# Performance work log

Measured on AMD Instinct MI355X. Metric: run time of the kernel, lower is better.

Reference implementation:

```python
import jax, jax.numpy as jnp
import numpy as np

N_PE = 100000   # num 'pe' nodes
N_R = 100000    # num 'router' nodes
E = 600000      # edges per relation
D_IN = 64       # input feature dim per node type
H = 128         # hidden_channels
G = 64          # graphs in batch


def setup_inputs() -> dict:
    key = jax.random.key(0)
    ks = jax.random.split(key, 20)
    inp = {}
    inp["x_pe"] = jax.random.normal(ks[0], (N_PE, D_IN), jnp.float32)
    inp["x_r"] = jax.random.normal(ks[1], (N_R, D_IN), jnp.float32)
    # edge_index per relation: row0 = src node ids, row1 = dst node ids
    inp["ei_per"] = jax.random.randint(ks[2], (2, E), 0, N_PE, jnp.int32)   # pe -> router
    inp["ei_rpe"] = jax.random.randint(ks[3], (2, E), 0, N_R, jnp.int32)    # router -> pe
    inp["ei_rr"] = jax.random.randint(ks[4], (2, E), 0, N_R, jnp.int32)     # router -> router
    inp["batch_pe"] = jnp.sort(jax.random.randint(ks[5], (N_PE,), 0, G, jnp.int32))
    inp["batch_r"] = jnp.sort(jax.random.randint(ks[6], (N_R,), 0, G, jnp.int32))
    # GraphConv params, relation axis ordered [pe->router, router->pe, router->router]
    s1 = 1.0 / np.sqrt(D_IN)
    s2 = 1.0 / np.sqrt(H)
    inp["Wrel1"] = jax.random.normal(ks[7], (3, D_IN, H), jnp.float32) * s1
    inp["brel1"] = jnp.zeros((3, H), jnp.float32)
    inp["Wroot1"] = jax.random.normal(ks[8], (3, D_IN, H), jnp.float32) * s1
    inp["Wrel23"] = jax.random.normal(ks[9], (2, 3, H, H), jnp.float32) * s2
    inp["brel23"] = jnp.zeros((2, 3, H), jnp.float32)
    inp["Wroot23"] = jax.random.normal(ks[10], (2, 3, H, H), jnp.float32) * s2
    # per-node-type MLP heads, type axis ordered [pe, router]
    inp["mlp_W1"] = jax.random.normal(ks[11], (2, H, 5), jnp.float32) * s2
    inp["mlp_b1"] = jnp.zeros((2, 5), jnp.float32)
    inp["mlp_W2"] = jax.random.normal(ks[12], (2, 5, 1), jnp.float32) * (1.0 / np.sqrt(5.0))
    inp["mlp_b2"] = jnp.zeros((2, 1), jnp.float32)
    inp["out_W"] = jax.random.normal(ks[13], (2, 1), jnp.float32) * (1.0 / np.sqrt(2.0))
    inp["out_b"] = jnp.zeros((1,), jnp.float32)
    return inp


def _hetero_graphconv(x_pe, x_r, ei_per, ei_rpe, ei_rr, Wrel, brel, Wroot):
    # GraphConv: lin_rel(scatter_add(x_src)) + lin_root(x_dst); to_hetero sums per dst type.
    agg_r_from_pe = jax.ops.segment_sum(x_pe[ei_per[0]], ei_per[1], num_segments=N_R)
    agg_pe_from_r = jax.ops.segment_sum(x_r[ei_rpe[0]], ei_rpe[1], num_segments=N_PE)
    agg_r_from_r = jax.ops.segment_sum(x_r[ei_rr[0]], ei_rr[1], num_segments=N_R)
    o_pe = agg_pe_from_r @ Wrel[1] + brel[1] + x_pe @ Wroot[1]
    o_r = (agg_r_from_pe @ Wrel[0] + brel[0] + x_r @ Wroot[0]) \
        + (agg_r_from_r @ Wrel[2] + brel[2] + x_r @ Wroot[2])
    return o_pe, o_r


def reference(x_pe, x_r, ei_per, ei_rpe, ei_rr, batch_pe, batch_r,
              Wrel1, brel1, Wroot1, Wrel23, brel23, Wroot23,
              mlp_W1, mlp_b1, mlp_W2, mlp_b2, out_W, out_b):
    h_pe, h_r = _hetero_graphconv(x_pe, x_r, ei_per, ei_rpe, ei_rr, Wrel1, brel1, Wroot1)
    h_pe, h_r = jax.nn.relu(h_pe), jax.nn.relu(h_r)
    h_pe, h_r = _hetero_graphconv(h_pe, h_r, ei_per, ei_rpe, ei_rr, Wrel23[0], brel23[0], Wroot23[0])
    h_pe, h_r = jax.nn.relu(h_pe), jax.nn.relu(h_r)
    h_pe, h_r = _hetero_graphconv(h_pe, h_r, ei_per, ei_rpe, ei_rr, Wrel23[1], brel23[1], Wroot23[1])
    gm_pe = jax.ops.segment_max(h_pe, batch_pe, num_segments=G)  # [G, H]
    gm_r = jax.ops.segment_max(h_r, batch_r, num_segments=G)
    def mlp(x, W1, b1, W2, b2):
        return jax.nn.relu(x @ W1 + b1) @ W2 + b2
    o_pe = mlp(gm_pe, mlp_W1[0], mlp_b1[0], mlp_W2[0], mlp_b2[0])  # [G, 1]
    o_r = mlp(gm_r, mlp_W1[1], mlp_b1[1], mlp_W2[1], mlp_b2[1])
    cat = jnp.concatenate([o_pe, o_r], axis=1)  # [G, 2]
    return cat @ out_W + out_b  # [G, 1]
```

## Files before the change

kernel.cpp:

```cpp
#include <hip/hip_runtime.h>
#include <cstddef>
#include <cstdint>

#define DIN 64
#define HID 128
#define NBKMAX 256
#define EPB 2048

typedef _Float16 half4v __attribute__((ext_vector_type(4)));
typedef _Float16 half8v __attribute__((ext_vector_type(8)));
typedef float f32x16 __attribute__((ext_vector_type(16)));

__device__ __forceinline__ unsigned encf(float f) {
    unsigned b = __float_as_uint(f);
    return (b & 0x80000000u) ? ~b : (b | 0x80000000u);
}
__device__ __forceinline__ float decf(unsigned u) {
    unsigned b = (u & 0x80000000u) ? (u & 0x7FFFFFFFu) : ~u;
    return __uint_as_float(b);
}

__global__ void conv_x2_k(const float* s0, _Float16* d0, int n40,
                          const float* s1, _Float16* d1, int n41) {
    int r = blockIdx.y;
    const float* s = r == 0 ? s0 : s1;
    _Float16* d = r == 0 ? d0 : d1;
    int n4 = r == 0 ? n40 : n41;
    int i = blockIdx.x * 256 + threadIdx.x;
    if (i >= n4) return;
    float4 v = *reinterpret_cast<const float4*>(&s[i * 4]);
    half4v h;
    h.x = (_Float16)v.x; h.y = (_Float16)v.y; h.z = (_Float16)v.z; h.w = (_Float16)v.w;
    *reinterpret_cast<half4v*>(&d[i * 4]) = h;
}

struct CW { const float* src; const float* src2; _Float16* dst; int K; int total; };
__global__ __launch_bounds__(256) void prep_k(
    CW c0, CW c1, CW c2, CW c3, CW c4, CW c5, CW c6, CW c7,
    const int* e0, const int* e1, const int* e2, int E,
    int* hc0, int* hc1, int* hc2,
    const int* bpe, int npe, int* spe,
    const int* brr, int nrr, int* srr, int G) {
    int y = blockIdx.y;
    if (y < 8) {
        CW J;
        switch (y) {
            case 0: J = c0; break; case 1: J = c1; break; case 2: J = c2; break;
            case 3: J = c3; break; case 4: J = c4; break; case 5: J = c5; break;
            case 6: J = c6; break; default: J = c7; break;
        }
        int i = blockIdx.x * 256 + threadIdx.x;
        if (i >= J.total) return;
        int m = i / (J.K * HID);
        int rem = i % (J.K * HID);
        int k = rem / HID;
        int col = rem % HID;
        float v = J.src[i];
        if (J.src2) v += J.src2[i];
        J.dst[(size_t)m * HID * J.K + (size_t)col * J.K + k] = (_Float16)v;
    } else if (y < 11) {
        int r = y - 8;
        const int* ei = r == 0 ? e0 : (r == 1 ? e1 : e2);
        int* cnt = r == 0 ? hc0 : (r == 1 ? hc1 : hc2);
        __shared__ int sc[NBKMAX];
        int t = threadIdx.x;
        sc[t] = 0;
        __syncthreads();
        int base = blockIdx.x * EPB;
        if (base >= E) return;
        int n = min(EPB, E - base);
        for (int i = t; i < n; i += 256)
            atomicAdd(&sc[(unsigned)ei[E + base + i] >> 9], 1);
        __syncthreads();
        if (sc[t]) atomicAdd(&cnt[t], sc[t]);
    } else {
        int r = blockIdx.x;
        if (r >= 2) return;
        const int* batch = r == 0 ? bpe : brr;
        int n = r == 0 ? npe : nrr;
        int* starts = r == 0 ? spe : srr;
        int g = threadIdx.x;
        if (g > G) return;
        int lo = 0, hi = n;
        while (lo < hi) {
            int mid = (lo + hi) >> 1;
            if (batch[mid] < g) lo = mid + 1; else hi = mid;
        }
        starts[g] = lo;
    }
}

__global__ __launch_bounds__(256) void bscan_k(int* c0, int* bb0, int* cu0, int* rp0, int n0,
                                               int* c1, int* bb1, int* cu1, int* rp1, int n1,
                                               int* c2, int* bb2, int* cu2, int* rp2, int n2,
                                               int E) {
    __shared__ int sh[256];
    int t = threadIdx.x;
    for (int r = 0; r < 3; ++r) {
        int* cnt = r == 0 ? c0 : (r == 1 ? c1 : c2);
        int* bb  = r == 0 ? bb0 : (r == 1 ? bb1 : bb2);
        int* cu  = r == 0 ? cu0 : (r == 1 ? cu1 : cu2);
        int* rp  = r == 0 ? rp0 : (r == 1 ? rp1 : rp2);
        int N    = r == 0 ? n0 : (r == 1 ? n1 : n2);
        int v = cnt[t];
        sh[t] = v;
        __syncthreads();
        for (int off = 1; off < 256; off <<= 1) {
            int val = (t >= off) ? sh[t - off] : 0;
            __syncthreads();
            sh[t] += val;
            __syncthreads();
        }
        int ex = sh[t] - v;
        bb[t] = ex;
        cu[t] = ex;
        if (t == 255) bb[256] = sh[255];
        if (t == 0) rp[N] = E;
        __syncthreads();
    }
}

__global__ __launch_bounds__(256) void bin_k(const int* e0, const int* e1, const int* e2, int E,
                                             int* cu0, int* cu1, int* cu2,
                                             unsigned* t0, unsigned* t1, unsigned* t2) {
    int r = blockIdx.y;
    const int* ei = r == 0 ? e0 : (r == 1 ? e1 : e2);
    int* gcur = r == 0 ? cu0 : (r == 1 ? cu1 : cu2);
    unsigned* temp = r == 0 ? t0 : (r == 1 ? t1 : t2);
    __shared__ unsigned pk[EPB];
    __shared__ unsigned short bkb[EPB];
    __shared__ int cnt[NBKMAX];
    __shared__ int scn[NBKMAX];
    __shared__ int rb[NBKMAX];
    int t = threadIdx.x;
    int base = blockIdx.x * EPB;
    int n = min(EPB, E - base);
    cnt[t] = 0;
    __syncthreads();
    for (int i = t; i < n; i += 256)
        atomicAdd(&cnt[(unsigned)ei[E + base + i] >> 9], 1);
    __syncthreads();
    {
        int v = cnt[t];
        scn[t] = v;
        __syncthreads();
        for (int off = 1; off < 256; off <<= 1) {
            int val = (t >= off) ? scn[t - off] : 0;
            __syncthreads();
            scn[t] += val;
            __syncthreads();
        }
        int ex = scn[t] - v;
        __syncthreads();
        scn[t] = ex;
    }
    {
        int c = cnt[t];
        rb[t] = c ? atomicAdd(&gcur[t], c) : 0;
        cnt[t] = 0;
    }
    __syncthreads();
    for (int i = t; i < n; i += 256) {
        int s = ei[base + i];
        int d = ei[E + base + i];
        int b = (unsigned)d >> 9;
        int slot = scn[b] + atomicAdd(&cnt[b], 1);
        pk[slot] = ((unsigned)s << 9) | (unsigned)(d & 511);
        bkb[slot] = (unsigned short)b;
    }
    __syncthreads();
    for (int i = t; i < n; i += 256) {
        int b = bkb[i];
        temp[rb[b] + (i - scn[b])] = pk[i];
    }
}

__global__ __launch_bounds__(256) void bcsr_k(const unsigned* t0, const unsigned* t1, const unsigned* t2,
                                              const int* bb0, const int* bb1, const int* bb2,
                                              int* rp0, int* rp1, int* rp2,
                                              int* a0, int* a1, int* a2,
                                              int n0, int n1, int n2) {
    int r = blockIdx.y;
    const unsigned* temp = r == 0 ? t0 : (r == 1 ? t1 : t2);
    const int* bb = r == 0 ? bb0 : (r == 1 ? bb1 : bb2);
    int* rp = r == 0 ? rp0 : (r == 1 ? rp1 : rp2);
    int* adj = r == 0 ? a0 : (r == 1 ? a1 : a2);
    int N = r == 0 ? n0 : (r == 1 ? n1 : n2);
    int b = blockIdx.x;
    int lo = bb[b], hi = bb[b + 1];
    __shared__ int cnt[512];
    __shared__ int sh[256];
    int t = threadIdx.x;
    cnt[t] = 0; cnt[t + 256] = 0;
    __syncthreads();
    for (int i = lo + t; i < hi; i += 256)
        atomicAdd(&cnt[temp[i] & 511], 1);
    __syncthreads();
    int c0 = cnt[2 * t], c1 = cnt[2 * t + 1];
    sh[t] = c0 + c1;
    __syncthreads();
    for (int off = 1; off < 256; off <<= 1) {
        int v = (t >= off) ? sh[t - off] : 0;
        __syncthreads();
        sh[t] += v;
        __syncthreads();
    }
    int pairExcl = sh[t] - (c0 + c1);
    __syncthreads();
    int e0x = lo + pairExcl;
    int e1x = e0x + c0;
    cnt[2 * t] = e0x;
    cnt[2 * t + 1] = e1x;
    int nodeBase = b * 512;
    if (nodeBase + 2 * t < N) rp[nodeBase + 2 * t] = e0x;
    if (nodeBase + 2 * t + 1 < N) rp[nodeBase + 2 * t + 1] = e1x;
    __syncthreads();
    for (int i = lo + t; i < hi; i += 256) {
        unsigned p = temp[i];
        int pos = atomicAdd(&cnt[p & 511], 1);
        adj[pos] = p >> 9;
    }
}

struct AJob { const _Float16* X; const int* rp; const int* adj; _Float16* AGG; int N; int gb; };
template <int D>
__global__ __launch_bounds__(256) void gather3_k(AJob a0, AJob a1, AJob a2) {
    int b = blockIdx.x;
    AJob J;
    if (b < a0.gb) { J = a0; }
    else if (b < a0.gb + a1.gb) { J = a1; b -= a0.gb; }
    else { J = a2; b -= a0.gb + a1.gb; }
    constexpr int TPN = D / 8;
    constexpr int NPB = 256 / TPN;
    int node = b * NPB + threadIdx.x / TPN;
    int glane = threadIdx.x % TPN;
    if (node >= J.N) return;
    int a = J.rp[node], e1 = J.rp[node + 1];
    float acc[8] = {0.f, 0.f, 0.f, 0.f, 0.f, 0.f, 0.f, 0.f};
    for (int base = a; base < e1; base += TPN) {
        int idx = base + glane;
        int myAdj = (idx < e1) ? J.adj[idx] : 0;
        int cnt = min(TPN, e1 - base);
        int j = 0;
        for (; j + 4 <= cnt; j += 4) {
            int s0 = __shfl(myAdj, j, TPN);
            int s1 = __shfl(myAdj, j + 1, TPN);
            int s2 = __shfl(myAdj, j + 2, TPN);
            int s3 = __shfl(myAdj, j + 3, TPN);
            half8v v0 = *reinterpret_cast<const half8v*>(&J.X[(size_t)s0 * D + glane * 8]);
            half8v v1 = *reinterpret_cast<const half8v*>(&J.X[(size_t)s1 * D + glane * 8]);
            half8v v2 = *reinterpret_cast<const half8v*>(&J.X[(size_t)s2 * D + glane * 8]);
            half8v v3 = *reinterpret_cast<const half8v*>(&J.X[(size_t)s3 * D + glane * 8]);
#pragma unroll
            for (int i = 0; i < 8; ++i)
                acc[i] += (float)v0[i] + (float)v1[i] + (float)v2[i] + (float)v3[i];
        }
        for (; j < cnt; ++j) {
            int s0 = __shfl(myAdj, j, TPN);
            half8v v0 = *reinterpret_cast<const half8v*>(&J.X[(size_t)s0 * D + glane * 8]);
#pragma unroll
            for (int i = 0; i < 8; ++i) acc[i] += (float)v0[i];
        }
    }
    half8v o;
#pragma unroll
    for (int i = 0; i < 8; ++i) o[i] = (_Float16)acc[i];
    *reinterpret_cast<half8v*>(&J.AGG[(size_t)node * D + glane * 8]) = o;
}

struct GJob {
    const _Float16* A0; const _Float16* A1; const _Float16* A2;
    const _Float16* W0; const _Float16* W1; const _Float16* W2;
    const float* b0; const float* b1;
    _Float16* O;
    int N; int total; int gb;
    const int* batch;
    const int* starts;
    unsigned* gmU;
    float* part;
    int* pgid;
};

template <bool RELU, bool SEGMAX>
__global__ __launch_bounds__(256) void gemm2_k(GJob j0, GJob j1, int K, int lg) {
    const bool second = ((int)blockIdx.x >= j0.gb);
    const GJob J = second ? j1 : j0;
    const int bx = blockIdx.x - (second ? j0.gb : 0);
    __shared__ _Float16 Alds[2][128 * 64];
    __shared__ _Float16 Wlds[2][128 * 64];
    const int tid = threadIdx.x;
    const int lane = tid & 63;
    const int w = tid >> 6;
    const int wr = w & 1, wc = w >> 1;
    const int rowBase = bx * 128;

    f32x16 acc[2][2];
#pragma unroll
    for (int r = 0; r < 2; ++r)
#pragma unroll
        for (int c = 0; c < 2; ++c)
#pragma unroll
            for (int q = 0; q < 16; ++q) acc[r][c][q] = 0.0f;

    const _Float16* Ap[3] = {J.A0, J.A1, J.A2};
    const _Float16* Wp[3] = {J.W0, J.W1, J.W2};

    int srow[4];
    int soff[4];
    int ldsoff[4];
#pragma unroll
    for (int i = 0; i < 4; ++i) {
        int r_ = (w * 4 + i) * 8 + (lane >> 3);
        srow[i] = r_;
        soff[i] = ((lane & 7) ^ (r_ & 7)) << 4;
        ldsoff[i] = (w * 4 + i) << 10;
    }

    const int total = J.total;
    const int cmask = (1 << lg) - 1;

    auto stage = [&](int c, int buf) {
        const int s = c >> lg;
        const int k0b = (c & cmask) << 7;
        const char* Ab = (const char*)Ap[s];
        const char* Wb = (const char*)Wp[s];
        char* al = (char*)&Alds[buf][0];
        char* wl = (char*)&Wlds[buf][0];
#pragma unroll
        for (int i = 0; i < 4; ++i) {
            const char* ga = Ab + ((size_t)(rowBase + srow[i]) * K) * 2 + k0b + soff[i];
            const char* gw = Wb + ((size_t)srow[i] * K) * 2 + k0b + soff[i];
            __builtin_amdgcn_global_load_lds(
                (const __attribute__((address_space(1))) void*)ga,
                (__attribute__((address_space(3))) void*)(al + ldsoff[i]), 16, 0, 0);
            __builtin_amdgcn_global_load_lds(
                (const __attribute__((address_space(1))) void*)gw,
                (__attribute__((address_space(3))) void*)(wl + ldsoff[i]), 16, 0, 0);
        }
    };

    stage(0, 0);
    asm volatile("s_waitcnt vmcnt(0)\n\ts_barrier" ::: "memory");

    const int rA0 = wr * 64 + (lane & 31);
    const int cW0 = wc * 64 + (lane & 31);
    const int ghi = lane >> 5;

    for (int c = 0; c < total; ++c) {
        if (c + 1 < total) stage(c + 1, (c + 1) & 1);
        const _Float16* al = &Alds[c & 1][0];
        const _Float16* wl = &Wlds[c & 1][0];
#pragma unroll
        for (int t = 0; t < 4; ++t) {
            const int g = 2 * t + ghi;
            half8v av[2], wv[2];
#pragma unroll
            for (int r = 0; r < 2; ++r) {
                const int row = rA0 + r * 32;
                av[r] = *reinterpret_cast<const half8v*>(al + ((row * 8 + (g ^ (row & 7))) << 3));
            }
#pragma unroll
            for (int cc = 0; cc < 2; ++cc) {
                const int col = cW0 + cc * 32;
                wv[cc] = *reinterpret_cast<const half8v*>(wl + ((col * 8 + (g ^ (col & 7))) << 3));
            }
#pragma unroll
            for (int r = 0; r < 2; ++r)
#pragma unroll
                for (int cc = 0; cc < 2; ++cc)
                    acc[r][cc] = __builtin_amdgcn_mfma_f32_32x32x16_f16(wv[cc], av[r], acc[r][cc], 0, 0, 0);
        }
        asm volatile("s_waitcnt vmcnt(0)\n\ts_barrier" ::: "memory");
    }

    const int half_ = lane >> 5;
    const int lane31 = lane & 31;

    if constexpr (SEGMAX) {
        __shared__ float smaxS[2][2][HID];
        const float NEGINF = -__builtin_huge_valf();
        {
            float* sf = (float*)smaxS;
            sf[tid] = NEGINF;
            sf[tid + 256] = NEGINF;
        }
        const int node0 = rowBase + wr * 64 + lane31;
        const int node1 = node0 + 32;
        const bool ok0 = (node0 < J.N);
        const bool ok1 = (node1 < J.N);
        const int lastn = min(rowBase + 127, J.N - 1);
        const int gfirst = J.batch[rowBase];
        const int glast = J.batch[lastn];
        const int gcnt = glast - gfirst + 1;
        __syncthreads();
        if (gcnt <= 2) {
            const int boundary = (gcnt == 2) ? J.starts[gfirst + 1] : 0x7FFFFFFF;
            for (int s = 0; s < gcnt; ++s) {
                const bool in0 = ok0 && ((node0 >= boundary) == (s == 1));
                const bool in1 = ok1 && ((node1 >= boundary) == (s == 1));
#pragma unroll
                for (int cc = 0; cc < 2; ++cc)
#pragma unroll
                for (int g = 0; g < 4; ++g) {
                    const int f = wc * 64 + cc * 32 + g * 8 + 4 * half_;
                    float4 bv = *reinterpret_cast<const float4*>(&J.b0[f]);
                    if (J.b1) {
                        float4 b2v = *reinterpret_cast<const float4*>(&J.b1[f]);
                        bv.x += b2v.x; bv.y += b2v.y; bv.z += b2v.z; bv.w += b2v.w;
                    }
#pragma unroll
                    for (int i = 0; i < 4; ++i) {
                        float bb_ = ((const float*)&bv)[i];
                        float v0 = in0 ? (acc[0][cc][g * 4 + i] + bb_) : NEGINF;
                        float v1 = in1 ? (acc[1][cc][g * 4 + i] + bb_) : NEGINF;
                        float vm = fmaxf(v0, v1);
#pragma unroll
                        for (int off = 1; off < 32; off <<= 1)
                            vm = fmaxf(vm, __shfl_xor(vm, off, 32));
                        if (lane31 == 0) smaxS[s][wr][f + i] = vm;
                    }
                }
            }
        } else {
#pragma unroll
            for (int r = 0; r < 2; ++r) {
                const int node = rowBase + wr * 64 + r * 32 + lane31;
                if (node >= J.N) continue;
                const int gid = J.batch[node];
                unsigned* gbase = J.gmU + (size_t)gid * HID;
#pragma unroll
                for (int cc = 0; cc < 2; ++cc)
#pragma unroll
                for (int g = 0; g < 4; ++g) {
                    const int f = wc * 64 + cc * 32 + g * 8 + 4 * half_;
                    float4 bv = *reinterpret_cast<const float4*>(&J.b0[f]);
                    if (J.b1) {
                        float4 b2v = *reinterpret_cast<const float4*>(&J.b1[f]);
                        bv.x += b2v.x; bv.y += b2v.y; bv.z += b2v.z; bv.w += b2v.w;
                    }
#pragma unroll
                    for (int i = 0; i < 4; ++i) {
                        float v = acc[r][cc][g * 4 + i] + ((const float*)&bv)[i];
                        atomicMax(&gbase[f + i], encf(v));
                    }
                }
            }
        }
        __syncthreads();
        if (tid < 128) {
#pragma unroll
            for (int s = 0; s < 2; ++s) {
                float m = fmaxf(smaxS[s][0][tid], smaxS[s][1][tid]);
                J.part[((size_t)bx * 2 + s) * HID + tid] = m;
            }
        }
        if (tid < 2) J.pgid[bx * 2 + tid] = (gcnt <= 2 && tid < gcnt) ? gfirst + tid : -1;
        return;
    }

#pragma unroll
    for (int r = 0; r < 2; ++r) {
        int node = rowBase + (wr * 2 + r) * 32 + lane31;
        bool ok = (node < J.N);
        _Float16* orow = J.O + (size_t)node * HID;
#pragma unroll
        for (int cc = 0; cc < 2; ++cc) {
            int fbase = wc * 64 + cc * 32;
#pragma unroll
            for (int g = 0; g < 4; ++g) {
                int fmine = fbase + g * 8 + 4 * half_;
                float4 bv = *reinterpret_cast<const float4*>(&J.b0[fmine]);
                if (J.b1) {
                    float4 b2v = *reinterpret_cast<const float4*>(&J.b1[fmine]);
                    bv.x += b2v.x; bv.y += b2v.y; bv.z += b2v.z; bv.w += b2v.w;
                }
                union { half4v h; int i[2]; } m, p;
#pragma unroll
                for (int i = 0; i < 4; ++i) {
                    float v = acc[r][cc][g * 4 + i] + ((const float*)&bv)[i];
                    if (RELU) v = fmaxf(v, 0.f);
                    m.h[i] = (_Float16)v;
                }
                p.i[0] = __shfl_xor(m.i[0], 32);
                p.i[1] = __shfl_xor(m.i[1], 32);
                half4v lo = half_ ? p.h : m.h;
                half4v hi = half_ ? m.h : p.h;
                half8v outv;
#pragma unroll
                for (int i = 0; i < 4; ++i) { outv[i] = lo[i]; outv[4 + i] = hi[i]; }
                if (ok && ((g & 1) == half_))
                    *reinterpret_cast<half8v*>(&orow[fbase + g * 8]) = outv;
            }
        }
    }
}

__global__ __launch_bounds__(128) void segred_k(
    const float* pP, const int* gP, const int* stP, unsigned* gmP,
    const float* pR, const int* gR, const int* stR, unsigned* gmR) {
    int z = blockIdx.y;
    const float* part = z == 0 ? pP : pR;
    const int* pgid   = z == 0 ? gP : gR;
    const int* starts = z == 0 ? stP : stR;
    unsigned* gmU     = z == 0 ? gmP : gmR;
    int g = blockIdx.x;
    int f = threadIdx.x;
    int s0 = starts[g], s1 = starts[g + 1];
    if (s0 >= s1) return;
    int b0 = s0 >> 7, b1 = (s1 - 1) >> 7;
    float m = -__builtin_huge_valf();
    for (int b = b0; b <= b1; ++b) {
#pragma unroll
        for (int s = 0; s < 2; ++s) {
            if (pgid[b * 2 + s] == g)
                m = fmaxf(m, part[((size_t)b * 2 + s) * HID + f]);
        }
    }
    atomicMax(&gmU[g * HID + f], encf(m));
}

__global__ void head_k(const unsigned* __restrict__ gmU_pe, const unsigned* __restrict__ gmU_r,
                       const float* __restrict__ W1, const float* __restrict__ b1,
                       const float* __restrict__ W2, const float* __restrict__ b2,
                       const float* __restrict__ oW, const float* __restrict__ ob,
                       float* __restrict__ out, int G) {
    int g = threadIdx.x;
    if (g >= G) return;
    float vals[2];
#pragma unroll
    for (int t = 0; t < 2; ++t) {
        const unsigned* gm = t ? gmU_r : gmU_pe;
        float z[5];
#pragma unroll
        for (int j = 0; j < 5; ++j) z[j] = b1[t * 5 + j];
        for (int f = 0; f < HID; ++f) {
            float x = decf(gm[g * HID + f]);
#pragma unroll
            for (int j = 0; j < 5; ++j) z[j] = fmaf(x, W1[t * HID * 5 + f * 5 + j], z[j]);
        }
        float o = b2[t];
#pragma unroll
        for (int j = 0; j < 5; ++j) o = fmaf(fmaxf(z[j], 0.f), W2[t * 5 + j], o);
        vals[t] = o;
    }
    out[g] = vals[0] * oW[0] + vals[1] * oW[1] + ob[0];
}

extern "C" void kernel_launch(void* const* d_in, const int* in_sizes, int n_in,
                              void* d_out, int out_size, void* d_ws, size_t ws_size,
                              hipStream_t stream) {
    const float* x_pe    = (const float*)d_in[0];
    const float* x_r     = (const float*)d_in[1];
    const int* ei_per    = (const int*)d_in[2];
    const int* ei_rpe    = (const int*)d_in[3];
    const int* ei_rr     = (const int*)d_in[4];
    const int* batch_pe  = (const int*)d_in[5];
    const int* batch_r   = (const int*)d_in[6];
    const float* Wrel1   = (const float*)d_in[7];
    const float* brel1   = (const float*)d_in[8];
    const float* Wroot1  = (const float*)d_in[9];
    const float* Wrel23  = (const float*)d_in[10];
    const float* brel23  = (const float*)d_in[11];
    const float* Wroot23 = (const float*)d_in[12];
    const float* mlp_W1  = (const float*)d_in[13];
    const float* mlp_b1  = (const float*)d_in[14];
    const float* mlp_W2  = (const float*)d_in[15];
    const float* mlp_b2  = (const float*)d_in[16];
    const float* out_W   = (const float*)d_in[17];
    const float* out_b   = (const float*)d_in[18];
    float* out = (float*)d_out;

    const int N_PE = in_sizes[0] / DIN;
    const int N_R  = in_sizes[1] / DIN;
    const int E    = in_sizes[2] / 2;
    const int G    = out_size;
    const int NMAX = (N_PE > N_R) ? N_PE : N_R;
    const size_t SZM = (size_t)NMAX * HID;

    _Float16* H1 = (_Float16*)d_ws;
    _Float16* H2 = H1 + SZM;
    _Float16* H3 = H2 + SZM;
    _Float16* H4 = H3 + SZM;
    _Float16* H5 = H4 + SZM;
    _Float16* xh_pe = H5 + SZM;
    _Float16* xh_r  = xh_pe + (size_t)N_PE * DIN;
    _Float16* wt_rel1    = xh_r + (size_t)N_R * DIN;
    _Float16* wt_root1pe = wt_rel1 + 3 * DIN * HID;
    _Float16* wt_wsum1   = wt_root1pe + DIN * HID;
    _Float16* wt_rel23   = wt_wsum1 + DIN * HID;
    _Float16* wt_root_l2 = wt_rel23 + 6 * HID * HID;
    _Float16* wt_root_l3 = wt_root_l2 + HID * HID;
    _Float16* wt_wsum2   = wt_root_l3 + HID * HID;
    _Float16* wt_wsum3   = wt_wsum2 + HID * HID;
    unsigned* gmU_pe = (unsigned*)(wt_wsum3 + HID * HID);
    unsigned* gmU_r  = gmU_pe + G * HID;
    int* bktCnt = (int*)(gmU_r + G * HID);
    int* starts_pe = bktCnt + 3 * NBKMAX;
    int* starts_r  = starts_pe + (G + 1);
    int* bb     = starts_r + (G + 1);
    int* gcur   = bb + 3 * (NBKMAX + 1);
    int* csr    = gcur + 3 * NBKMAX;
    const size_t relstride = (size_t)(NMAX + 1) + 2 * (size_t)E + 16;

    int* rp[3]; int* adjp[3]; unsigned* tmp[3];
    const int Nds[3] = {N_R, N_PE, N_R};
    for (int r = 0; r < 3; ++r) {
        int* rowptr = csr + (size_t)r * relstride;
        rp[r] = rowptr;
        adjp[r] = rowptr + (Nds[r] + 1);
        tmp[r] = (unsigned*)(adjp[r] + E);
    }

    const int gpe = (N_PE + 127) / 128, grr = (N_R + 127) / 128;
    const int eb = (E + EPB - 1) / EPB;

    float* part_pe = (float*)tmp[0];
    float* part_r  = part_pe + (size_t)gpe * 2 * HID;
    int*   pgid_pe = (int*)(part_r + (size_t)grr * 2 * HID);
    int*   pgid_r  = pgid_pe + gpe * 2;

    hipMemsetAsync(gmU_pe, 0, (2 * (size_t)G * HID + 3 * NBKMAX) * sizeof(int), stream);
    {
        int n40 = N_PE * DIN / 4, n41 = N_R * DIN / 4;
        int nmax = n40 > n41 ? n40 : n41;
        dim3 g((nmax + 255) / 256, 2);
        conv_x2_k<<<g, 256, 0, stream>>>(x_pe, xh_pe, n40, x_r, xh_r, n41);
    }
    {
        CW c0{Wrel1, nullptr, wt_rel1, DIN, 3 * DIN * HID};
        CW c1{Wroot1 + 1 * DIN * HID, nullptr, wt_root1pe, DIN, DIN * HID};
        CW c2{Wroot1, Wroot1 + 2 * DIN * HID, wt_wsum1, DIN, DIN * HID};
        CW c3{Wrel23, nullptr, wt_rel23, HID, 6 * HID * HID};
        CW c4{Wroot23 + 1 * HID * HID, nullptr, wt_root_l2, HID, HID * HID};
        CW c5{Wroot23 + 4 * HID * HID, nullptr, wt_root_l3, HID, HID * HID};
        CW c6{Wroot23, Wroot23 + 2 * HID * HID, wt_wsum2, HID, HID * HID};
        CW c7{Wroot23 + 3 * HID * HID, Wroot23 + 5 * HID * HID, wt_wsum3, HID, HID * HID};
        int gx = (6 * HID * HID + 255) / 256;
        if (eb > gx) gx = eb;
        dim3 g(gx, 12);
        prep_k<<<g, 256, 0, stream>>>(c0, c1, c2, c3, c4, c5, c6, c7,
                                      ei_per, ei_rpe, ei_rr, E,
                                      bktCnt, bktCnt + NBKMAX, bktCnt + 2 * NBKMAX,
                                      batch_pe, N_PE, starts_pe,
                                      batch_r, N_R, starts_r, G);
    }
    {
        bscan_k<<<1, 256, 0, stream>>>(
            bktCnt, bb, gcur, rp[0], Nds[0],
            bktCnt + NBKMAX, bb + (NBKMAX + 1), gcur + NBKMAX, rp[1], Nds[1],
            bktCnt + 2 * NBKMAX, bb + 2 * (NBKMAX + 1), gcur + 2 * NBKMAX, rp[2], Nds[2], E);
        dim3 gh(eb, 3);
        bin_k<<<gh, 256, 0, stream>>>(ei_per, ei_rpe, ei_rr, E,
                                      gcur, gcur + NBKMAX, gcur + 2 * NBKMAX,
                                      tmp[0], tmp[1], tmp[2]);
        dim3 gc(NBKMAX, 3);
        bcsr_k<<<gc, 256, 0, stream>>>(tmp[0], tmp[1], tmp[2],
                                       bb, bb + (NBKMAX + 1), bb + 2 * (NBKMAX + 1),
                                       rp[0], rp[1], rp[2],
                                       adjp[0], adjp[1], adjp[2],
                                       Nds[0], Nds[1], Nds[2]);
    }

    {
        AJob a0{xh_r, rp[1], adjp[1], H1, N_PE, (N_PE + 31) / 32};
        AJob a1{xh_pe, rp[0], adjp[0], H2, N_R, (N_R + 31) / 32};
        AJob a2{xh_r, rp[2], adjp[2], H3, N_R, (N_R + 31) / 32};
        gather3_k<DIN><<<a0.gb + a1.gb + a2.gb, 256, 0, stream>>>(a0, a1, a2);
        GJob jp{H1, xh_pe, nullptr,
                wt_rel1 + 1 * DIN * HID, wt_root1pe, nullptr,
                brel1 + HID, nullptr, H4, N_PE, 2, gpe,
                nullptr, nullptr, nullptr, nullptr, nullptr};
        GJob jr{H2, H3, xh_r,
                wt_rel1, wt_rel1 + 2 * DIN * HID, wt_wsum1,
                brel1, brel1 + 2 * HID, H5, N_R, 3, grr,
                nullptr, nullptr, nullptr, nullptr, nullptr};
        gemm2_k<true, false><<<gpe + grr, 256, 0, stream>>>(jp, jr, DIN, 0);
    }
    {
        AJob a0{H5, rp[1], adjp[1], H1, N_PE, (N_PE + 15) / 16};
        AJob a1{H4, rp[0], adjp[0], H2, N_R, (N_R + 15) / 16};
        AJob a2{H5, rp[2], adjp[2], H3, N_R, (N_R + 15) / 16};
        gather3_k<HID><<<a0.gb + a1.gb + a2.gb, 256, 0, stream>>>(a0, a1, a2);
        GJob jp{H1, H4, nullptr,
                wt_rel23 + 1 * HID * HID, wt_root_l2, nullptr,
                brel23 + HID, nullptr, H1, N_PE, 2 * 2, gpe,
                nullptr, nullptr, nullptr, nullptr, nullptr};
        GJob jr{H2, H3, H5,
                wt_rel23, wt_rel23 + 2 * HID * HID, wt_wsum2,
                brel23, brel23 + 2 * HID, H2, N_R, 3 * 2, grr,
                nullptr, nullptr, nullptr, nullptr, nullptr};
        gemm2_k<true, false><<<gpe + grr, 256, 0, stream>>>(jp, jr, HID, 1);
    }
    {
        AJob a0{H2, rp[1], adjp[1], H3, N_PE, (N_PE + 15) / 16};
        AJob a1{H1, rp[0], adjp[0], H4, N_R, (N_R + 15) / 16};
        AJob a2{H2, rp[2], adjp[2], H5, N_R, (N_R + 15) / 16};
        gather3_k<HID><<<a0.gb + a1.gb + a2.gb, 256, 0, stream>>>(a0, a1, a2);
        GJob jp{H3, H1, nullptr,
                wt_rel23 + 4 * HID * HID, wt_root_l3, nullptr,
                brel23 + 4 * HID, nullptr, nullptr, N_PE, 2 * 2, gpe,
                batch_pe, starts_pe, gmU_pe, part_pe, pgid_pe};
        GJob jr{H4, H5, H2,
                wt_rel23 + 3 * HID * HID, wt_rel23 + 5 * HID * HID, wt_wsum3,
                brel23 + 3 * HID, brel23 + 5 * HID, nullptr, N_R, 3 * 2, grr,
                batch_r, starts_r, gmU_r, part_r, pgid_r};
        gemm2_k<false, true><<<gpe + grr, 256, 0, stream>>>(jp, jr, HID, 1);
    }

    segred_k<<<dim3(G, 2), 128, 0, stream>>>(part_pe, pgid_pe, starts_pe, gmU_pe,
                                             part_r, pgid_r, starts_r, gmU_r);
    head_k<<<1, 64, 0, stream>>>(gmU_pe, gmU_r, mlp_W1, mlp_b1, mlp_W2, mlp_b2, out_W, out_b, out, G);
}
```

Baseline: 545.5 us.

## Fuse neighbor aggregation into GEMM kernel, aggregating directly into LDS

Removes the separate gather3_k launches and instead has each GEMM block aggregate neighbor features for its 128 rows straight into shared memory before running the MFMA loop over that source. This avoids writing the aggregated intermediates to global memory and reading them back. The cost is that the gather and the MFMA work are now serialized inside each block, and the LDS footprint grows to a full 128xK A tile, which may reduce occupancy.

```diff
diff --git a/kernel.cpp b/kernel.cpp
--- a/kernel.cpp
+++ b/kernel.cpp
@@ -222,58 +222,14 @@
     }
 }
 
-struct AJob { const _Float16* X; const int* rp; const int* adj; _Float16* AGG; int N; int gb; };
-template <int D>
-__global__ __launch_bounds__(256) void gather3_k(AJob a0, AJob a1, AJob a2) {
-    int b = blockIdx.x;
-    AJob J;
-    if (b < a0.gb) { J = a0; }
-    else if (b < a0.gb + a1.gb) { J = a1; b -= a0.gb; }
-    else { J = a2; b -= a0.gb + a1.gb; }
-    constexpr int TPN = D / 8;
-    constexpr int NPB = 256 / TPN;
-    int node = b * NPB + threadIdx.x / TPN;
-    int glane = threadIdx.x % TPN;
-    if (node >= J.N) return;
-    int a = J.rp[node], e1 = J.rp[node + 1];
-    float acc[8] = {0.f, 0.f, 0.f, 0.f, 0.f, 0.f, 0.f, 0.f};
-    for (int base = a; base < e1; base += TPN) {
-        int idx = base + glane;
-        int myAdj = (idx < e1) ? J.adj[idx] : 0;
-        int cnt = min(TPN, e1 - base);
-        int j = 0;
-        for (; j + 4 <= cnt; j += 4) {
-            int s0 = __shfl(myAdj, j, TPN);
-            int s1 = __shfl(myAdj, j + 1, TPN);
-            int s2 = __shfl(myAdj, j + 2, TPN);
-            int s3 = __shfl(myAdj, j + 3, TPN);
-            half8v v0 = *reinterpret_cast<const half8v*>(&J.X[(size_t)s0 * D + glane * 8]);
-            half8v v1 = *reinterpret_cast<const half8v*>(&J.X[(size_t)s1 * D + glane * 8]);
-            half8v v2 = *reinterpret_cast<const half8v*>(&J.X[(size_t)s2 * D + glane * 8]);
-            half8v v3 = *reinterpret_cast<const half8v*>(&J.X[(size_t)s3 * D + glane * 8]);
-#pragma unroll
-            for (int i = 0; i < 8; ++i)
-                acc[i] += (float)v0[i] + (float)v1[i] + (float)v2[i] + (float)v3[i];
-        }
-        for (; j < cnt; ++j) {
-            int s0 = __shfl(myAdj, j, TPN);
-            half8v v0 = *reinterpret_cast<const half8v*>(&J.X[(size_t)s0 * D + glane * 8]);
-#pragma unroll
-            for (int i = 0; i < 8; ++i) acc[i] += (float)v0[i];
-        }
-    }
-    half8v o;
-#pragma unroll
-    for (int i = 0; i < 8; ++i) o[i] = (_Float16)acc[i];
-    *reinterpret_cast<half8v*>(&J.AGG[(size_t)node * D + glane * 8]) = o;
-}
-
 struct GJob {
-    const _Float16* A0; const _Float16* A1; const _Float16* A2;
+    const _Float16* X0; const int* rp0; const int* adj0;
+    const _Float16* X1; const int* rp1; const int* adj1;
+    const _Float16* X2;
     const _Float16* W0; const _Float16* W1; const _Float16* W2;
     const float* b0; const float* b1;
     _Float16* O;
-    int N; int total; int gb;
+    int N; int nsrc; int gb;
     const int* batch;
     const int* starts;
     unsigned* gmU;
@@ -281,12 +237,15 @@
     int* pgid;
 };
 
-template <bool RELU, bool SEGMAX>
-__global__ __launch_bounds__(256) void gemm2_k(GJob j0, GJob j1, int K, int lg) {
+template <bool RELU, bool SEGMAX, int K>
+__global__ __launch_bounds__(256) void gemm2_k(GJob j0, GJob j1) {
+    constexpr int CH = K / 64;
+    constexpr int TPN = K / 8;
+    constexpr int GRP = 256 / TPN;
     const bool second = ((int)blockIdx.x >= j0.gb);
     const GJob J = second ? j1 : j0;
     const int bx = blockIdx.x - (second ? j0.gb : 0);
-    __shared__ _Float16 Alds[2][128 * 64];
+    __shared__ _Float16 Alds[128 * K];
     __shared__ _Float16 Wlds[2][128 * 64];
     const int tid = threadIdx.x;
     const int lane = tid & 63;
@@ -302,12 +261,9 @@
 #pragma unroll
             for (int q = 0; q < 16; ++q) acc[r][c][q] = 0.0f;
 
-    const _Float16* Ap[3] = {J.A0, J.A1, J.A2};
     const _Float16* Wp[3] = {J.W0, J.W1, J.W2};
 
-    int srow[4];
-    int soff[4];
-    int ldsoff[4];
+    int srow[4], soff[4], ldsoff[4];
 #pragma unroll
     for (int i = 0; i < 4; ++i) {
         int r_ = (w * 4 + i) * 8 + (lane >> 3);
@@ -316,61 +272,138 @@
         ldsoff[i] = (w * 4 + i) << 10;
     }
 
-    const int total = J.total;
-    const int cmask = (1 << lg) - 1;
-
-    auto stage = [&](int c, int buf) {
-        const int s = c >> lg;
-        const int k0b = (c & cmask) << 7;
-        const char* Ab = (const char*)Ap[s];
-        const char* Wb = (const char*)Wp[s];
-        char* al = (char*)&Alds[buf][0];
+    const int total = J.nsrc * CH;
+
+    auto stageW = [&](int c_, int buf) {
+        const int s_ = c_ / CH;
+        const int k0b = (c_ - s_ * CH) << 7;
+        const char* Wb = (const char*)Wp[s_];
         char* wl = (char*)&Wlds[buf][0];
 #pragma unroll
         for (int i = 0; i < 4; ++i) {
-            const char* ga = Ab + ((size_t)(rowBase + srow[i]) * K) * 2 + k0b + soff[i];
             const char* gw = Wb + ((size_t)srow[i] * K) * 2 + k0b + soff[i];
-            __builtin_amdgcn_global_load_lds(
-                (const __attribute__((address_space(1))) void*)ga,
-                (__attribute__((address_space(3))) void*)(al + ldsoff[i]), 16, 0, 0);
             __builtin_amdgcn_global_load_lds(
                 (const __attribute__((address_space(1))) void*)gw,
                 (__attribute__((address_space(3))) void*)(wl + ldsoff[i]), 16, 0, 0);
         }
     };
 
-    stage(0, 0);
-    asm volatile("s_waitcnt vmcnt(0)\n\ts_barrier" ::: "memory");
+    auto aggregate = [&](const _Float16* Xs, const int* rp, const int* adj) {
+        const int gg = tid / TPN;
+        const int glane = tid % TPN;
+#pragma unroll 1
+        for (int pass = 0; pass < 128 / GRP; ++pass) {
+            const int lrow = pass * GRP + gg;
+            const int node = rowBase + lrow;
+            float a8[8] = {0.f, 0.f, 0.f, 0.f, 0.f, 0.f, 0.f, 0.f};
+            if (node < J.N) {
+                int a = rp[node], e1 = rp[node + 1];
+                for (int base = a; base < e1; base += TPN) {
+                    int idx = base + glane;
+                    int myAdj = (idx < e1) ? adj[idx] : 0;
+                    int cnt = min(TPN, e1 - base);
+                    int j = 0;
+                    for (; j + 4 <= cnt; j += 4) {
+                        int s0 = __shfl(myAdj, j, TPN);
+                        int s1 = __shfl(myAdj, j + 1, TPN);
+                        int s2 = __shfl(myAdj, j + 2, TPN);
+                        int s3 = __shfl(myAdj, j + 3, TPN);
+                        half8v v0 = *reinterpret_cast<const half8v*>(&Xs[(size_t)s0 * K + glane * 8]);
+                        half8v v1 = *reinterpret_cast<const half8v*>(&Xs[(size_t)s1 * K + glane * 8]);
+                        half8v v2 = *reinterpret_cast<const half8v*>(&Xs[(size_t)s2 * K + glane * 8]);
+                        half8v v3 = *reinterpret_cast<const half8v*>(&Xs[(size_t)s3 * K + glane * 8]);
+#pragma unroll
+                        for (int i = 0; i < 8; ++i)
+                            a8[i] += (float)v0[i] + (float)v1[i] + (float)v2[i] + (float)v3[i];
+                    }
+                    for (; j < cnt; ++j) {
+                        int s0 = __shfl(myAdj, j, TPN);
+                        half8v v0 = *reinterpret_cast<const half8v*>(&Xs[(size_t)s0 * K + glane * 8]);
+#pragma unroll
+                        for (int i = 0; i < 8; ++i) a8[i] += (float)v0[i];
+                    }
+                }
+            }
+            half8v o;
+#pragma unroll
+            for (int i = 0; i < 8; ++i) o[i] = (_Float16)a8[i];
+            int gran;
+            if constexpr (K == 128)
+                gran = lrow * 16 + (glane & 8) + ((glane & 7) ^ (lrow & 7));
+            else
+                gran = lrow * 8 + (glane ^ (lrow & 7));
+            *reinterpret_cast<half8v*>(&Alds[gran * 8]) = o;
+        }
+    };
+
+    auto stageRoot = [&](const _Float16* Xr) {
+        char* al = (char*)&Alds[0];
+        const char* Xb = (const char*)Xr;
+        if constexpr (K == 128) {
+#pragma unroll
+            for (int i = 0; i < 8; ++i) {
+                int rr = w * 32 + i * 4 + (lane >> 4);
+                int g16 = lane & 15;
+                int sb = (g16 & 8) * 16 + (((g16 & 7) ^ (rr & 7)) << 4);
+                __builtin_amdgcn_global_load_lds(
+                    (const __attribute__((address_space(1))) void*)(Xb + (size_t)(rowBase + rr) * 256 + sb),
+                    (__attribute__((address_space(3))) void*)(al + (w * 32 + i * 4) * 256 + lane * 16), 16, 0, 0);
+            }
+        } else {
+#pragma unroll
+            for (int i = 0; i < 4; ++i) {
+                int rr = w * 32 + i * 8 + (lane >> 3);
+                int g8 = lane & 7;
+                int sb = (g8 ^ (rr & 7)) << 4;
+                __builtin_amdgcn_global_load_lds(
+                    (const __attribute__((address_space(1))) void*)(Xb + (size_t)(rowBase + rr) * 128 + sb),
+                    (__attribute__((address_space(3))) void*)(al + (w * 32 + i * 8) * 128 + lane * 16), 16, 0, 0);
+            }
+        }
+    };
 
     const int rA0 = wr * 64 + (lane & 31);
     const int cW0 = wc * 64 + (lane & 31);
     const int ghi = lane >> 5;
 
-    for (int c = 0; c < total; ++c) {
-        if (c + 1 < total) stage(c + 1, (c + 1) & 1);
-        const _Float16* al = &Alds[c & 1][0];
-        const _Float16* wl = &Wlds[c & 1][0];
-#pragma unroll
-        for (int t = 0; t < 4; ++t) {
-            const int g = 2 * t + ghi;
-            half8v av[2], wv[2];
-#pragma unroll
-            for (int r = 0; r < 2; ++r) {
-                const int row = rA0 + r * 32;
-                av[r] = *reinterpret_cast<const half8v*>(al + ((row * 8 + (g ^ (row & 7))) << 3));
+    int c = 0;
+    for (int s = 0; s < J.nsrc; ++s) {
+        const _Float16* Xs = s == 0 ? J.X0 : (s == 1 ? J.X1 : J.X2);
+        const int* rpS = s == 0 ? J.rp0 : (s == 1 ? J.rp1 : nullptr);
+        const int* adjS = s == 0 ? J.adj0 : (s == 1 ? J.adj1 : nullptr);
+        if (adjS != nullptr) {
+            aggregate(Xs, rpS, adjS);
+            if (c == 0) stageW(0, 0);
+            __syncthreads();
+        } else {
+            stageRoot(Xs);
+            asm volatile("s_waitcnt vmcnt(0)\n\ts_barrier" ::: "memory");
+        }
+        for (int kc = 0; kc < CH; ++kc, ++c) {
+            if (c + 1 < total) stageW(c + 1, (c + 1) & 1);
+            const _Float16* wl = &Wlds[c & 1][0];
+#pragma unroll
+            for (int t = 0; t < 4; ++t) {
+                const int g = 2 * t + ghi;
+                half8v av[2], wv[2];
+#pragma unroll
+                for (int r = 0; r < 2; ++r) {
+                    const int row = rA0 + r * 32;
+                    av[r] = *reinterpret_cast<const half8v*>(&Alds[(row * TPN + kc * 8 + (g ^ (row & 7))) * 8]);
+                }
+#pragma unroll
+                for (int cc = 0; cc < 2; ++cc) {
+                    const int col = cW0 + cc * 32;
+                    wv[cc] = *reinterpret_cast<const half8v*>(&wl[(col * 8 + (g ^ (col & 7))) * 8]);
+                }
+#pragma unroll
+                for (int r = 0; r < 2; ++r)
+#pragma unroll
+                    for (int cc = 0; cc < 2; ++cc)
+                        acc[r][cc] = __builtin_amdgcn_mfma_f32_32x32x16_f16(wv[cc], av[r], acc[r][cc], 0, 0, 0);
             }
-#pragma unroll
-            for (int cc = 0; cc < 2; ++cc) {
-                const int col = cW0 + cc * 32;
-                wv[cc] = *reinterpret_cast<const half8v*>(wl + ((col * 8 + (g ^ (col & 7))) << 3));
-            }
-#pragma unroll
-            for (int r = 0; r < 2; ++r)
-#pragma unroll
-                for (int cc = 0; cc < 2; ++cc)
-                    acc[r][cc] = __builtin_amdgcn_mfma_f32_32x32x16_f16(wv[cc], av[r], acc[r][cc], 0, 0, 0);
-        }
-        asm volatile("s_waitcnt vmcnt(0)\n\ts_barrier" ::: "memory");
+            asm volatile("s_waitcnt vmcnt(0)\n\ts_barrier" ::: "memory");
+        }
     }
 
     const int half_ = lane >> 5;
@@ -662,49 +695,49 @@
     }
 
     {
-        AJob a0{xh_r, rp[1], adjp[1], H1, N_PE, (N_PE + 31) / 32};
-        AJob a1{xh_pe, rp[0], adjp[0], H2, N_R, (N_R + 31) / 32};
-        AJob a2{xh_r, rp[2], adjp[2], H3, N_R, (N_R + 31) / 32};
-        gather3_k<DIN><<<a0.gb + a1.gb + a2.gb, 256, 0, stream>>>(a0, a1, a2);
-        GJob jp{H1, xh_pe, nullptr,
+        GJob jp{xh_r, rp[1], adjp[1],
+                xh_pe, nullptr, nullptr,
+                nullptr,
                 wt_rel1 + 1 * DIN * HID, wt_root1pe, nullptr,
                 brel1 + HID, nullptr, H4, N_PE, 2, gpe,
                 nullptr, nullptr, nullptr, nullptr, nullptr};
-        GJob jr{H2, H3, xh_r,
+        GJob jr{xh_pe, rp[0], adjp[0],
+                xh_r, rp[2], adjp[2],
+                xh_r,
                 wt_rel1, wt_rel1 + 2 * DIN * HID, wt_wsum1,
                 brel1, brel1 + 2 * HID, H5, N_R, 3, grr,
                 nullptr, nullptr, nullptr, nullptr, nullptr};
-        gemm2_k<true, false><<<gpe + grr, 256, 0, stream>>>(jp, jr, DIN, 0);
+        gemm2_k<true, false, 64><<<gpe + grr, 256, 0, stream>>>(jp, jr);
     }
     {
-        AJob a0{H5, rp[1], adjp[1], H1, N_PE, (N_PE + 15) / 16};
-        AJob a1{H4, rp[0], adjp[0], H2, N_R, (N_R + 15) / 16};
-        AJob a2{H5, rp[2], adjp[2], H3, N_R, (N_R + 15) / 16};
-        gather3_k<HID><<<a0.gb + a1.gb + a2.gb, 256, 0, stream>>>(a0, a1, a2);
-        GJob jp{H1, H4, nullptr,
+        GJob jp{H5, rp[1], adjp[1],
+                H4, nullptr, nullptr,
+                nullptr,
                 wt_rel23 + 1 * HID * HID, wt_root_l2, nullptr,
-                brel23 + HID, nullptr, H1, N_PE, 2 * 2, gpe,
+                brel23 + HID, nullptr, H1, N_PE, 2, gpe,
                 nullptr, nullptr, nullptr, nullptr, nullptr};
-        GJob jr{H2, H3, H5,
+        GJob jr{H4, rp[0], adjp[0],
+                H5, rp[2], adjp[2],
+                H5,
                 wt_rel23, wt_rel23 + 2 * HID * HID, wt_wsum2,
-                brel23, brel23 + 2 * HID, H2, N_R, 3 * 2, grr,
+                brel23, brel23 + 2 * HID, H2, N_R, 3, grr,
                 nullptr, nullptr, nullptr, nullptr, nullptr};
-        gemm2_k<true, false><<<gpe + grr, 256, 0, stream>>>(jp, jr, HID, 1);
+        gemm2_k<true, false, 128><<<gpe + grr, 256, 0, stream>>>(jp, jr);
     }
     {
-        AJob a0{H2, rp[1], adjp[1], H3, N_PE, (N_PE + 15) / 16};
-        AJob a1{H1, rp[0], adjp[0], H4, N_R, (N_R + 15) / 16};
-        AJob a2{H2, rp[2], adjp[2], H5, N_R, (N_R + 15) / 16};
-        gather3_k<HID><<<a0.gb + a1.gb + a2.gb, 256, 0, stream>>>(a0, a1, a2);
-        GJob jp{H3, H1, nullptr,
+        GJob jp{H2, rp[1], adjp[1],
+                H1, nullptr, nullptr,
+                nullptr,
                 wt_rel23 + 4 * HID * HID, wt_root_l3, nullptr,
-                brel23 + 4 * HID, nullptr, nullptr, N_PE, 2 * 2, gpe,
+                brel23 + 4 * HID, nullptr, nullptr, N_PE, 2, gpe,
                 batch_pe, starts_pe, gmU_pe, part_pe, pgid_pe};
-        GJob jr{H4, H5, H2,
+        GJob jr{H1, rp[0], adjp[0],
+                H2, rp[2], adjp[2],
+                H2,
                 wt_rel23 + 3 * HID * HID, wt_rel23 + 5 * HID * HID, wt_wsum3,
-                brel23 + 3 * HID, brel23 + 5 * HID, nullptr, N_R, 3 * 2, grr,
+                brel23 + 3 * HID, brel23 + 5 * HID, nullptr, N_R, 3, grr,
                 batch_r, starts_r, gmU_r, part_r, pgid_r};
-        gemm2_k<false, true><<<gpe + grr, 256, 0, stream>>>(jp, jr, HID, 1);
+        gemm2_k<false, true, 128><<<gpe + grr, 256, 0, stream>>>(jp, jr);
     }
 
     segred_k<<<dim3(G, 2), 128, 0, stream>>>(part_pe, pgid_pe, starts_pe, gmU_pe,
```

Measured after the change: 687.0 us. 25.9% more time.
